# Performance work log

Measured on AMD Instinct MI355X. Metric: run time of the kernel, lower is better.

Reference implementation:

```python
import jax, jax.numpy as jnp
import numpy as np

N_RAYS = 32768
HID = 64
MARCH_ITERS = 64
EPS = 1e-4
NEAR = 0.0
FAR = 1.0
T_FAR = 1.0
TPUT_B = 64
JITTER = 1.0 / TPUT_B  # fixed stand-in for random.random() * (2 / batch_size)


def _init_linear(key, fan_in, fan_out):
    kw, kb = jax.random.split(key)
    lim = 1.0 / np.sqrt(fan_in)
    W = jax.random.uniform(kw, (fan_in, fan_out), jnp.float32, -lim, lim)
    b = jax.random.uniform(kb, (fan_out,), jnp.float32, -lim, lim)
    return W, b


def setup_inputs() -> dict:
    key = jax.random.key(0)
    ks = jax.random.split(key, 6)
    rays = jax.random.normal(ks[0], (N_RAYS, 6), jnp.float32)
    W0, b0 = _init_linear(ks[1], 3, HID)
    W1, b1 = _init_linear(ks[2], HID, HID)
    W2, b2 = _init_linear(ks[3], HID, 1)
    Wr0, br0 = _init_linear(ks[4], 6, HID)
    Wr1, br1 = _init_linear(ks[5], HID, 3)
    return dict(rays=rays, W0=W0, b0=b0, W1=W1, b1=b1, W2=W2, b2=b2,
                Wr0=Wr0, br0=br0, Wr1=Wr1, br1=br1)


def _sdf(p, W0, b0, W1, b1, W2, b2):
    # p: [N, 3] -> signed distance [N, 1]
    h = jax.nn.relu(p @ W0 + b0)
    h = jax.nn.relu(h @ W1 + b1)
    return h @ W2 + b2


def _refl(p, d, Wr0, br0, Wr1, br1):
    # p, d: [N, 3] -> RGB [N, 3]
    h = jax.nn.relu(jnp.concatenate([p, d], axis=-1) @ Wr0 + br0)
    return jax.nn.sigmoid(h @ Wr1 + br1)


def reference(rays, W0, b0, W1, b1, W2, b2, Wr0, br0, Wr1, br1):
    r_o, r_d = rays[..., :3], rays[..., 3:]
    sdf = lambda p: _sdf(p, W0, b0, W1, b1, W2, b2)

    # --- sphere march (64 fixed iterations; early-exit break is a no-op
    # once all rays hit, since hit rays stop updating) ---
    hits0 = jnp.zeros(r_o.shape[:-1] + (1,), jnp.bool_)
    dist0 = jnp.full(r_o.shape[:-1] + (1,), NEAR, jnp.float32)

    def march(carry, _):
        hits, cd = carry
        d = sdf(r_o + r_d * cd)  # [N, 1]
        hits = hits | ((d < EPS) & (cd >= NEAR) & (cd <= FAR))
        cd = jnp.where(~hits, cd + d, cd)
        return (hits, cd), None

    (hit, t), _ = jax.lax.scan(march, (hits0, dist0), None, length=MARCH_ITERS)
    pts = r_o + r_d * t

    rgb = _refl(pts, r_d, Wr0, br0, Wr1, br1)
    rgb = jnp.where(hit, rgb, 0.0)  # out[~hit] = 0

    # --- throughput (index search under no_grad in the original) ---
    max_t = T_FAR + JITTER
    step = max_t / TPUT_B
    sg = jax.lax.stop_gradient
    sdf_ng = lambda p: _sdf(p, sg(W0), sg(b0), sg(W1), sg(b1), sg(W2), sg(b2))
    r_o_ng, r_d_ng = sg(r_o), sg(r_d)

    curr_min0 = sdf_ng(r_o_ng)[..., 0]          # [N]
    idxs0 = jnp.zeros_like(curr_min0, jnp.int32)

    def tloop(carry, i):
        cm, idxs = carry
        t_i = step * (i + 1).astype(jnp.float32)
        sd = sdf_ng(r_o_ng + t_i * r_d_ng)[..., 0]
        idxs = jnp.where(sd < cm, i + 1, idxs)
        return (jnp.minimum(cm, sd), idxs), None

    (_, idxs), _ = jax.lax.scan(tloop, (curr_min0, idxs0),
                                jnp.arange(TPUT_B, dtype=jnp.int32))

    best_pos = r_o + idxs[..., None].astype(jnp.float32) * step * r_d  # [N, 3]
    tput = sdf(best_pos)  # [N, 1], differentiable (outside no_grad in torch)

    return jnp.concatenate([rgb, tput], axis=-1)  # [N, 4]
```

## Files before the change

### kernel.cpp

```cpp
#include <hip/hip_runtime.h>
#include <math.h>

#define NRAYS        32768
#define MARCH_ITERS  64
#define EPS_         1e-4f
#define STEP_        ((1.0f + 1.0f/64.0f) / 64.0f)

typedef __attribute__((ext_vector_type(8)))  short    short8;
typedef __attribute__((ext_vector_type(4)))  float    float4v;
typedef __attribute__((ext_vector_type(2)))  float    float2v;
typedef __attribute__((ext_vector_type(4)))  unsigned uint4v;
typedef __attribute__((ext_vector_type(2)))  unsigned uint2v;

__device__ __forceinline__ short8 mk_frag(unsigned p0, unsigned p1,
                                          unsigned p2, unsigned p3) {
    uint4v v = {p0, p1, p2, p3};
    return __builtin_bit_cast(short8, v);
}

__device__ __forceinline__ unsigned packbf(unsigned a, unsigned b) {
    return __builtin_amdgcn_perm(b, a, 0x07060302u);
}

struct Split2 { unsigned h, r; };
__device__ __forceinline__ Split2 split2(float x) {
    unsigned xu = __float_as_uint(x);
    float xh = __uint_as_float(xu & 0xFFFF0000u);
    float rr = x - xh;
    return { xu, __float_as_uint(rr) };
}

__device__ __forceinline__ float2v fma2(float2v a, float2v b, float2v c) {
    return __builtin_elementwise_fma(a, b, c);
}

__device__ __forceinline__ float xor16_sum(float x) {
#if __has_builtin(__builtin_amdgcn_permlane16_swap)
    unsigned u = __float_as_uint(x);
    uint2v r = __builtin_amdgcn_permlane16_swap(u, u, false, false);
    return __uint_as_float(r.x) + __uint_as_float(r.y);
#else
    float p = __int_as_float(
        __builtin_amdgcn_ds_swizzle(__float_as_int(x), 0x401F));
    return x + p;
#endif
}
__device__ __forceinline__ float xor32_sum(float x) {
#if __has_builtin(__builtin_amdgcn_permlane32_swap)
    unsigned u = __float_as_uint(x);
    uint2v r = __builtin_amdgcn_permlane32_swap(u, u, false, false);
    return __uint_as_float(r.x) + __uint_as_float(r.y);
#else
    return x + __shfl_xor(x, 32, 64);
#endif
}

__global__ __launch_bounds__(64)
__attribute__((amdgpu_waves_per_eu(2, 8)))
void sdf_w16_k(
    const float* __restrict__ rays,
    const float* __restrict__ W0,  const float* __restrict__ b0,
    const float* __restrict__ W1,  const float* __restrict__ b1,
    const float* __restrict__ W2,  const float* __restrict__ b2,
    const float* __restrict__ Wr0, const float* __restrict__ br0,
    const float* __restrict__ Wr1, const float* __restrict__ br1,
    float* __restrict__ out)
{
    const int lane = threadIdx.x;
    const int quad = lane >> 4;
    const int m    = lane & 15;
    const int rayBase = blockIdx.x * 16;

    const float* rp = rays + (rayBase + m) * 6;
    const float ox = rp[0], oy = rp[1], oz = rp[2];
    const float dx = rp[3], dy = rp[4], dz = rp[5];

    float2v a2[4][2], s2[4][2];
    #pragma unroll
    for (int t = 0; t < 4; ++t)
        #pragma unroll
        for (int p = 0; p < 2; ++p) {
            float av[2], sv[2];
            #pragma unroll
            for (int e = 0; e < 2; ++e) {
                int j = 32 * (t >> 1) + 8 * quad + 4 * (t & 1) + (2 * p + e);
                float w0c = W0[j], w1c = W0[64 + j], w2c = W0[128 + j];
                av[e] = fmaf(ox, w0c, fmaf(oy, w1c, fmaf(oz, w2c, b0[j])));
                sv[e] = fmaf(dx, w0c, fmaf(dy, w1c, dz * w2c));
            }
            a2[t][p] = (float2v){av[0], av[1]};
            s2[t][p] = (float2v){sv[0], sv[1]};
        }

    float4v b1v[4];
    float2v w2a[4], w2b[4];
    #pragma unroll
    for (int t = 0; t < 4; ++t) {
        int base = 16 * t + 4 * quad;
        b1v[t] = (float4v){b1[base], b1[base + 1], b1[base + 2], b1[base + 3]};
        w2a[t] = (float2v){W2[base], W2[base + 1]};
        w2b[t] = (float2v){W2[base + 2], W2[base + 3]};
    }
    const float b2s = b2[0];

    short8 A2h[2][4], A2m[2][4];
    #pragma unroll
    for (int h = 0; h < 2; ++h)
        #pragma unroll
        for (int t = 0; t < 4; ++t) {
            unsigned pm[4], ph[4];
            #pragma unroll
            for (int jp = 0; jp < 4; ++jp) {
                int k0 = 32 * h + quad * 8 + 2 * jp;
                int j2 = 16 * t + m;
                Split2 a = split2(W1[k0 * 64 + j2]);
                Split2 b = split2(W1[(k0 + 1) * 64 + j2]);
                pm[jp] = packbf(a.r, b.r);
                ph[jp] = packbf(a.h, b.h);
            }
            A2m[h][t] = mk_frag(pm[0], pm[1], pm[2], pm[3]);
            A2h[h][t] = mk_frag(ph[0], ph[1], ph[2], ph[3]);
        }

    const float2v z2 = {0.f, 0.f};
    auto front = [&](float cv, short8* BH, short8* BM) {
        const float2v c2 = {cv, cv};
        unsigned PH[4][2], PM[4][2];
        #pragma unroll
        for (int t = 0; t < 4; ++t) {
            float2v v01 = fma2(c2, s2[t][0], a2[t][0]);
            float2v v23 = fma2(c2, s2[t][1], a2[t][1]);
            v01 = __builtin_elementwise_max(v01, z2);
            v23 = __builtin_elementwise_max(v23, z2);
            unsigned u0 = __float_as_uint(v01.x), u1 = __float_as_uint(v01.y);
            unsigned u2 = __float_as_uint(v23.x), u3 = __float_as_uint(v23.y);
            PH[t][0] = packbf(u0, u1); PH[t][1] = packbf(u2, u3);
            float2v h01 = {__uint_as_float(u0 & 0xFFFF0000u),
                           __uint_as_float(u1 & 0xFFFF0000u)};
            float2v h23 = {__uint_as_float(u2 & 0xFFFF0000u),
                           __uint_as_float(u3 & 0xFFFF0000u)};
            float2v r01 = v01 - h01;
            float2v r23 = v23 - h23;
            PM[t][0] = packbf(__float_as_uint(r01.x), __float_as_uint(r01.y));
            PM[t][1] = packbf(__float_as_uint(r23.x), __float_as_uint(r23.y));
        }
        #pragma unroll
        for (int h = 0; h < 2; ++h) {
            BH[h] = mk_frag(PH[2 * h][0], PH[2 * h][1],
                            PH[2 * h + 1][0], PH[2 * h + 1][1]);
            BM[h] = mk_frag(PM[2 * h][0], PM[2 * h][1],
                            PM[2 * h + 1][0], PM[2 * h + 1][1]);
        }
    };

    auto l3 = [&](const float4v* C2) -> float {
        float2v q01 = {0.f, 0.f}, q23 = {0.f, 0.f};
        #pragma unroll
        for (int t = 0; t < 4; ++t) {
            float2v rel01 = __builtin_elementwise_max(
                (float2v){C2[t][0], C2[t][1]}, z2);
            float2v rel23 = __builtin_elementwise_max(
                (float2v){C2[t][2], C2[t][3]}, z2);
            q01 = fma2(rel01, w2a[t], q01);
            q23 = fma2(rel23, w2b[t], q23);
        }
        float part = (q01.x + q01.y) + (q23.x + q23.y);
        part = xor16_sum(part);
        part = xor32_sum(part);
        return b2s + part;
    };

    auto tputC2 = [&](const short8* BHt, const short8* BMt, float4v* C2t) {
        #pragma unroll
        for (int t = 0; t < 4; ++t)
            C2t[t] = __builtin_amdgcn_mfma_f32_16x16x32_bf16(
                A2h[0][t], BMt[0], b1v[t], 0, 0, 0);
        #pragma unroll
        for (int t = 0; t < 4; ++t)
            C2t[t] = __builtin_amdgcn_mfma_f32_16x16x32_bf16(
                A2h[1][t], BMt[1], C2t[t], 0, 0, 0);
        #pragma unroll
        for (int h = 0; h < 2; ++h)
            #pragma unroll
            for (int t = 0; t < 4; ++t)
                C2t[t] = __builtin_amdgcn_mfma_f32_16x16x32_bf16(
                    A2h[h][t], BHt[h], C2t[t], 0, 0, 0);
    };

    bool  hit = false;
    float cd  = 0.f;
    float cm  = 3.4e38f;

    #pragma unroll 2
    for (int i = 0; i < MARCH_ITERS; ++i) {
        float ti = STEP_ * (float)i;
        short8 BHt[2], BMt[2];
        front(ti, BHt, BMt);
        short8 BHm[2], BMm[2];
        front(cd, BHm, BMm);
        float4v C2m[4], C2t[4];
        #pragma unroll
        for (int t = 0; t < 4; ++t)
            C2m[t] = __builtin_amdgcn_mfma_f32_16x16x32_bf16(
                A2m[0][t], BHm[0], b1v[t], 0, 0, 0);
        #pragma unroll
        for (int t = 0; t < 4; ++t)
            C2m[t] = __builtin_amdgcn_mfma_f32_16x16x32_bf16(
                A2m[1][t], BHm[1], C2m[t], 0, 0, 0);
        #pragma unroll
        for (int h = 0; h < 2; ++h)
            #pragma unroll
            for (int t = 0; t < 4; ++t)
                C2m[t] = __builtin_amdgcn_mfma_f32_16x16x32_bf16(
                    A2h[h][t], BMm[h], C2m[t], 0, 0, 0);
        #pragma unroll
        for (int h = 0; h < 2; ++h)
            #pragma unroll
            for (int t = 0; t < 4; ++t)
                C2m[t] = __builtin_amdgcn_mfma_f32_16x16x32_bf16(
                    A2h[h][t], BHm[h], C2m[t], 0, 0, 0);
        tputC2(BHt, BMt, C2t);
        float dm = l3(C2m);
        bool c = (dm < EPS_) && (cd >= 0.f) && (cd <= 1.f);
        hit = hit || c;
        if (!hit) cd += dm;
        cm = fminf(cm, l3(C2t));
    }

    {
        short8 BHt[2], BMt[2];
        front(STEP_ * 64.0f, BHt, BMt);
        float4v C2t[4];
        tputC2(BHt, BMt, C2t);
        cm = fminf(cm, l3(C2t));
    }

    const float px = fmaf(dx, cd, ox), py = fmaf(dy, cd, oy), pz = fmaf(dz, cd, oz);
    float r0 = 0.f, r1 = 0.f, r2 = 0.f;
    #pragma unroll 4
    for (int jj = 0; jj < 16; ++jj) {
        int j = quad * 16 + jj;
        float a = fmaf(px, Wr0[j],
                  fmaf(py, Wr0[64 + j],
                  fmaf(pz, Wr0[128 + j],
                  fmaf(dx, Wr0[192 + j],
                  fmaf(dy, Wr0[256 + j],
                  fmaf(dz, Wr0[320 + j], br0[j]))))));
        a = fmaxf(a, 0.f);
        r0 = fmaf(a, Wr1[j * 3 + 0], r0);
        r1 = fmaf(a, Wr1[j * 3 + 1], r1);
        r2 = fmaf(a, Wr1[j * 3 + 2], r2);
    }
    r0 = xor16_sum(r0); r0 = xor32_sum(r0);
    r1 = xor16_sum(r1); r1 = xor32_sum(r1);
    r2 = xor16_sum(r2); r2 = xor32_sum(r2);
    r0 = 1.f / (1.f + expf(-(r0 + br1[0])));
    r1 = 1.f / (1.f + expf(-(r1 + br1[1])));
    r2 = 1.f / (1.f + expf(-(r2 + br1[2])));
    if (!hit) { r0 = 0.f; r1 = 0.f; r2 = 0.f; }
    if (lane < 16) {
        float4v o4 = {r0, r1, r2, cm};
        *reinterpret_cast<float4v*>(out + (rayBase + lane) * 4) = o4;
    }
}

extern "C" void kernel_launch(void* const* d_in, const int* in_sizes, int n_in,
                              void* d_out, int out_size, void* d_ws, size_t ws_size,
                              hipStream_t stream) {
    const float* rays = (const float*)d_in[0];
    const float* W0   = (const float*)d_in[1];
    const float* b0   = (const float*)d_in[2];
    const float* W1   = (const float*)d_in[3];
    const float* b1   = (const float*)d_in[4];
    const float* W2   = (const float*)d_in[5];
    const float* b2   = (const float*)d_in[6];
    const float* Wr0  = (const float*)d_in[7];
    const float* br0  = (const float*)d_in[8];
    const float* Wr1  = (const float*)d_in[9];
    const float* br1  = (const float*)d_in[10];
    float* out = (float*)d_out;

    hipLaunchKernelGGL(sdf_w16_k, dim3(NRAYS / 16), dim3(64), 0, stream,
                       rays, W0, b0, W1, b1, W2, b2, Wr0, br0, Wr1, br1, out);
}
```

Before: 163.8 us.

## Process two 16-ray groups per wave to reuse weight fragments and add ILP

Each 64-thread wave now handles 32 rays as two 16-ray sub-batches that share the register-resident W1 MFMA fragments, halving the grid. The two independent MFMA chains per iteration are meant to hide MFMA and front-end latency through instruction-level parallelism instead of relying on multiple waves. Waves-per-EU is forced to 1 and the march loop is no longer unrolled, which raises the register budget but lowers occupancy and halves the number of blocks, so the GPU may be less well filled.

```diff
diff --git a/kernel.cpp b/kernel.cpp
--- a/kernel.cpp
+++ b/kernel.cpp
@@ -56,8 +56,8 @@
 }
 
 __global__ __launch_bounds__(64)
-__attribute__((amdgpu_waves_per_eu(2, 8)))
-void sdf_w16_k(
+__attribute__((amdgpu_waves_per_eu(1, 1)))
+void sdf_w17_k(
     const float* __restrict__ rays,
     const float* __restrict__ W0,  const float* __restrict__ b0,
     const float* __restrict__ W1,  const float* __restrict__ b1,
@@ -69,28 +69,36 @@
     const int lane = threadIdx.x;
     const int quad = lane >> 4;
     const int m    = lane & 15;
-    const int rayBase = blockIdx.x * 16;
-
-    const float* rp = rays + (rayBase + m) * 6;
-    const float ox = rp[0], oy = rp[1], oz = rp[2];
-    const float dx = rp[3], dy = rp[4], dz = rp[5];
-
-    float2v a2[4][2], s2[4][2];
-    #pragma unroll
-    for (int t = 0; t < 4; ++t)
-        #pragma unroll
-        for (int p = 0; p < 2; ++p) {
-            float av[2], sv[2];
-            #pragma unroll
-            for (int e = 0; e < 2; ++e) {
-                int j = 32 * (t >> 1) + 8 * quad + 4 * (t & 1) + (2 * p + e);
-                float w0c = W0[j], w1c = W0[64 + j], w2c = W0[128 + j];
-                av[e] = fmaf(ox, w0c, fmaf(oy, w1c, fmaf(oz, w2c, b0[j])));
-                sv[e] = fmaf(dx, w0c, fmaf(dy, w1c, dz * w2c));
+    const int rayBase = blockIdx.x * 32;
+
+    float oxA[2], oyA[2], ozA[2], dxA[2], dyA[2], dzA[2];
+    #pragma unroll
+    for (int s = 0; s < 2; ++s) {
+        const float* rp = rays + (rayBase + 16 * s + m) * 6;
+        oxA[s] = rp[0]; oyA[s] = rp[1]; ozA[s] = rp[2];
+        dxA[s] = rp[3]; dyA[s] = rp[4]; dzA[s] = rp[5];
+    }
+
+    float2v a2[2][4][2], s2[2][4][2];
+    #pragma unroll
+    for (int s = 0; s < 2; ++s)
+        #pragma unroll
+        for (int t = 0; t < 4; ++t)
+            #pragma unroll
+            for (int p = 0; p < 2; ++p) {
+                float av[2], sv[2];
+                #pragma unroll
+                for (int e = 0; e < 2; ++e) {
+                    int j = 32 * (t >> 1) + 8 * quad + 4 * (t & 1) + (2 * p + e);
+                    float w0c = W0[j], w1c = W0[64 + j], w2c = W0[128 + j];
+                    av[e] = fmaf(oxA[s], w0c,
+                            fmaf(oyA[s], w1c, fmaf(ozA[s], w2c, b0[j])));
+                    sv[e] = fmaf(dxA[s], w0c,
+                            fmaf(dyA[s], w1c, dzA[s] * w2c));
+                }
+                a2[s][t][p] = (float2v){av[0], av[1]};
+                s2[s][t][p] = (float2v){sv[0], sv[1]};
             }
-            a2[t][p] = (float2v){av[0], av[1]};
-            s2[t][p] = (float2v){sv[0], sv[1]};
-        }
 
     float4v b1v[4];
     float2v w2a[4], w2b[4];
@@ -123,13 +131,14 @@
         }
 
     const float2v z2 = {0.f, 0.f};
-    auto front = [&](float cv, short8* BH, short8* BM) {
+    auto front = [&](const float2v (&as)[4][2], const float2v (&ss)[4][2],
+                     float cv, short8* BH, short8* BM) {
         const float2v c2 = {cv, cv};
         unsigned PH[4][2], PM[4][2];
         #pragma unroll
         for (int t = 0; t < 4; ++t) {
-            float2v v01 = fma2(c2, s2[t][0], a2[t][0]);
-            float2v v23 = fma2(c2, s2[t][1], a2[t][1]);
+            float2v v01 = fma2(c2, ss[t][0], as[t][0]);
+            float2v v23 = fma2(c2, ss[t][1], as[t][1]);
             v01 = __builtin_elementwise_max(v01, z2);
             v23 = __builtin_elementwise_max(v23, z2);
             unsigned u0 = __float_as_uint(v01.x), u1 = __float_as_uint(v01.y);
@@ -170,6 +179,29 @@
         return b2s + part;
     };
 
+    auto marchC2 = [&](const short8* BHm, const short8* BMm, float4v* C2m) {
+        #pragma unroll
+        for (int t = 0; t < 4; ++t)
+            C2m[t] = __builtin_amdgcn_mfma_f32_16x16x32_bf16(
+                A2m[0][t], BHm[0], b1v[t], 0, 0, 0);
+        #pragma unroll
+        for (int t = 0; t < 4; ++t)
+            C2m[t] = __builtin_amdgcn_mfma_f32_16x16x32_bf16(
+                A2m[1][t], BHm[1], C2m[t], 0, 0, 0);
+        #pragma unroll
+        for (int h = 0; h < 2; ++h)
+            #pragma unroll
+            for (int t = 0; t < 4; ++t)
+                C2m[t] = __builtin_amdgcn_mfma_f32_16x16x32_bf16(
+                    A2h[h][t], BMm[h], C2m[t], 0, 0, 0);
+        #pragma unroll
+        for (int h = 0; h < 2; ++h)
+            #pragma unroll
+            for (int t = 0; t < 4; ++t)
+                C2m[t] = __builtin_amdgcn_mfma_f32_16x16x32_bf16(
+                    A2h[h][t], BHm[h], C2m[t], 0, 0, 0);
+    };
+
     auto tputC2 = [&](const short8* BHt, const short8* BMt, float4v* C2t) {
         #pragma unroll
         for (int t = 0; t < 4; ++t)
@@ -187,80 +219,79 @@
                     A2h[h][t], BHt[h], C2t[t], 0, 0, 0);
     };
 
-    bool  hit = false;
-    float cd  = 0.f;
-    float cm  = 3.4e38f;
-
-    #pragma unroll 2
+    bool  hit[2] = {false, false};
+    float cd[2]  = {0.f, 0.f};
+    float cm[2]  = {3.4e38f, 3.4e38f};
+
+    #pragma unroll 1
     for (int i = 0; i < MARCH_ITERS; ++i) {
         float ti = STEP_ * (float)i;
+        short8 BHt[2][2], BMt[2][2], BHm[2][2], BMm[2][2];
+        #pragma unroll
+        for (int s = 0; s < 2; ++s)
+            front(a2[s], s2[s], ti, BHt[s], BMt[s]);
+        #pragma unroll
+        for (int s = 0; s < 2; ++s)
+            front(a2[s], s2[s], cd[s], BHm[s], BMm[s]);
+        float4v C2m[2][4], C2t[2][4];
+        #pragma unroll
+        for (int s = 0; s < 2; ++s)
+            marchC2(BHm[s], BMm[s], C2m[s]);
+        #pragma unroll
+        for (int s = 0; s < 2; ++s)
+            tputC2(BHt[s], BMt[s], C2t[s]);
+        #pragma unroll
+        for (int s = 0; s < 2; ++s) {
+            float dm = l3(C2m[s]);
+            bool c = (dm < EPS_) && (cd[s] >= 0.f) && (cd[s] <= 1.f);
+            hit[s] = hit[s] || c;
+            if (!hit[s]) cd[s] += dm;
+        }
+        #pragma unroll
+        for (int s = 0; s < 2; ++s)
+            cm[s] = fminf(cm[s], l3(C2t[s]));
+    }
+
+    #pragma unroll
+    for (int s = 0; s < 2; ++s) {
         short8 BHt[2], BMt[2];
-        front(ti, BHt, BMt);
-        short8 BHm[2], BMm[2];
-        front(cd, BHm, BMm);
-        float4v C2m[4], C2t[4];
-        #pragma unroll
-        for (int t = 0; t < 4; ++t)
-            C2m[t] = __builtin_amdgcn_mfma_f32_16x16x32_bf16(
-                A2m[0][t], BHm[0], b1v[t], 0, 0, 0);
-        #pragma unroll
-        for (int t = 0; t < 4; ++t)
-            C2m[t] = __builtin_amdgcn_mfma_f32_16x16x32_bf16(
-                A2m[1][t], BHm[1], C2m[t], 0, 0, 0);
-        #pragma unroll
-        for (int h = 0; h < 2; ++h)
-            #pragma unroll
-            for (int t = 0; t < 4; ++t)
-                C2m[t] = __builtin_amdgcn_mfma_f32_16x16x32_bf16(
-                    A2h[h][t], BMm[h], C2m[t], 0, 0, 0);
-        #pragma unroll
-        for (int h = 0; h < 2; ++h)
-            #pragma unroll
-            for (int t = 0; t < 4; ++t)
-                C2m[t] = __builtin_amdgcn_mfma_f32_16x16x32_bf16(
-                    A2h[h][t], BHm[h], C2m[t], 0, 0, 0);
-        tputC2(BHt, BMt, C2t);
-        float dm = l3(C2m);
-        bool c = (dm < EPS_) && (cd >= 0.f) && (cd <= 1.f);
-        hit = hit || c;
-        if (!hit) cd += dm;
-        cm = fminf(cm, l3(C2t));
-    }
-
-    {
-        short8 BHt[2], BMt[2];
-        front(STEP_ * 64.0f, BHt, BMt);
+        front(a2[s], s2[s], STEP_ * 64.0f, BHt, BMt);
         float4v C2t[4];
         tputC2(BHt, BMt, C2t);
-        cm = fminf(cm, l3(C2t));
-    }
-
-    const float px = fmaf(dx, cd, ox), py = fmaf(dy, cd, oy), pz = fmaf(dz, cd, oz);
-    float r0 = 0.f, r1 = 0.f, r2 = 0.f;
-    #pragma unroll 4
-    for (int jj = 0; jj < 16; ++jj) {
-        int j = quad * 16 + jj;
-        float a = fmaf(px, Wr0[j],
-                  fmaf(py, Wr0[64 + j],
-                  fmaf(pz, Wr0[128 + j],
-                  fmaf(dx, Wr0[192 + j],
-                  fmaf(dy, Wr0[256 + j],
-                  fmaf(dz, Wr0[320 + j], br0[j]))))));
-        a = fmaxf(a, 0.f);
-        r0 = fmaf(a, Wr1[j * 3 + 0], r0);
-        r1 = fmaf(a, Wr1[j * 3 + 1], r1);
-        r2 = fmaf(a, Wr1[j * 3 + 2], r2);
-    }
-    r0 = xor16_sum(r0); r0 = xor32_sum(r0);
-    r1 = xor16_sum(r1); r1 = xor32_sum(r1);
-    r2 = xor16_sum(r2); r2 = xor32_sum(r2);
-    r0 = 1.f / (1.f + expf(-(r0 + br1[0])));
-    r1 = 1.f / (1.f + expf(-(r1 + br1[1])));
-    r2 = 1.f / (1.f + expf(-(r2 + br1[2])));
-    if (!hit) { r0 = 0.f; r1 = 0.f; r2 = 0.f; }
-    if (lane < 16) {
-        float4v o4 = {r0, r1, r2, cm};
-        *reinterpret_cast<float4v*>(out + (rayBase + lane) * 4) = o4;
+        cm[s] = fminf(cm[s], l3(C2t));
+    }
+
+    #pragma unroll
+    for (int s = 0; s < 2; ++s) {
+        const float px = fmaf(dxA[s], cd[s], oxA[s]);
+        const float py = fmaf(dyA[s], cd[s], oyA[s]);
+        const float pz = fmaf(dzA[s], cd[s], ozA[s]);
+        float r0 = 0.f, r1 = 0.f, r2 = 0.f;
+        #pragma unroll 4
+        for (int jj = 0; jj < 16; ++jj) {
+            int j = quad * 16 + jj;
+            float a = fmaf(px, Wr0[j],
+                      fmaf(py, Wr0[64 + j],
+                      fmaf(pz, Wr0[128 + j],
+                      fmaf(dxA[s], Wr0[192 + j],
+                      fmaf(dyA[s], Wr0[256 + j],
+                      fmaf(dzA[s], Wr0[320 + j], br0[j]))))));
+            a = fmaxf(a, 0.f);
+            r0 = fmaf(a, Wr1[j * 3 + 0], r0);
+            r1 = fmaf(a, Wr1[j * 3 + 1], r1);
+            r2 = fmaf(a, Wr1[j * 3 + 2], r2);
+        }
+        r0 = xor16_sum(r0); r0 = xor32_sum(r0);
+        r1 = xor16_sum(r1); r1 = xor32_sum(r1);
+        r2 = xor16_sum(r2); r2 = xor32_sum(r2);
+        r0 = 1.f / (1.f + expf(-(r0 + br1[0])));
+        r1 = 1.f / (1.f + expf(-(r1 + br1[1])));
+        r2 = 1.f / (1.f + expf(-(r2 + br1[2])));
+        if (!hit[s]) { r0 = 0.f; r1 = 0.f; r2 = 0.f; }
+        if (lane < 16) {
+            float4v o4 = {r0, r1, r2, cm[s]};
+            *reinterpret_cast<float4v*>(out + (rayBase + 16 * s + lane) * 4) = o4;
+        }
     }
 }
 
@@ -280,6 +311,6 @@
     const float* br1  = (const float*)d_in[10];
     float* out = (float*)d_out;
 
-    hipLaunchKernelGGL(sdf_w16_k, dim3(NRAYS / 16), dim3(64), 0, stream,
+    hipLaunchKernelGGL(sdf_w17_k, dim3(NRAYS / 32), dim3(64), 0, stream,
                        rays, W0, b0, W1, b1, W2, b2, Wr0, br0, Wr1, br1, out);
 }
```

Measured after the change: 172.0 us. 5.0% more time.
